# Kernel optimization log

Measured on AMD Instinct MI355X. Metric: run time of the kernel, lower is better.

Reference implementation:

```python
import jax, jax.numpy as jnp
import numpy as np

C = 128; HEADS = 4; DH = C // HEADS; R = 8; EPS = 1e-5; SCALE = DH ** -0.5
B = 1; H = 32; W = 32; D = 32


def _rel_index(r):
    # Faithful replication of RelativePositionBias index (incl. its quirks:
    # depth coord never offset, only coord0 scaled, negative indices wrap).
    coords = np.stack(np.meshgrid(np.arange(r), np.arange(r), np.arange(r), indexing='ij'))
    flat = coords.reshape(3, -1)
    rel = (flat[:, :, None] - flat[:, None, :]).transpose(1, 2, 0).astype(np.int64)
    rel[:, :, 0] += r - 1
    rel[:, :, 1] += r - 1
    rel[:, :, 0] *= 2 * r - 1
    idx = rel.sum(-1)
    tbl = (2 * r - 1) ** 3
    return np.where(idx < 0, idx + tbl, idx)  # torch-style negative index wrap

REL_IDX = jnp.array(_rel_index(R))  # [R^3, R^3]


def _interp_matrix(n_in, n_out):
    # 1-D linear interpolation matrix, align_corners=True (trilinear is separable)
    pos = np.arange(n_out) * (n_in - 1) / (n_out - 1)
    lo = np.clip(np.floor(pos).astype(np.int64), 0, n_in - 2)
    w = (pos - lo).astype(np.float32)
    M = np.zeros((n_out, n_in), np.float32)
    M[np.arange(n_out), lo] = 1.0 - w
    M[np.arange(n_out), lo + 1] += w
    return jnp.array(M)


def _conv3d(x, w, groups=1):
    ks = w.shape[-1]; p = ks // 2
    return jax.lax.conv_general_dilated(
        x, w, (1, 1, 1), ((p, p),) * 3,
        dimension_numbers=('NCDHW', 'OIDHW', 'NCDHW'),
        feature_group_count=groups)


def _bn(x, g, b):
    # training-mode BatchNorm3d: batch stats over (N, spatial), biased var
    mu = x.mean(axis=(0, 2, 3, 4), keepdims=True)
    var = x.var(axis=(0, 2, 3, 4), keepdims=True)
    return (x - mu) * jax.lax.rsqrt(var + EPS) * g.reshape(1, -1, 1, 1, 1) + b.reshape(1, -1, 1, 1, 1)


def _block(x, bn1_g, bn1_b, qkv_dw, qkv_pw, rel_table, out_dw, out_pw, bn2_g, bn2_b, mlp_w):
    Bx, Cx, Hx, Wx, Dx = x.shape
    h = _bn(x, bn1_g, bn1_b)
    qkv = _conv3d(_conv3d(h, qkv_dw, groups=C), qkv_pw)
    q, k, v = jnp.split(qkv, 3, axis=1)
    # trilinear downsample k, v to (R, R, R), align_corners=True
    Mh, Mw, Md = _interp_matrix(Hx, R), _interp_matrix(Wx, R), _interp_matrix(Dx, R)
    k = jnp.einsum('bchwd,ph,qw,rd->bcpqr', k, Mh, Mw, Md)
    v = jnp.einsum('bchwd,ph,qw,rd->bcpqr', v, Mh, Mw, Md)
    # channel layout is (dim_head, heads)
    q = q.reshape(Bx, DH, HEADS, Hx * Wx * Dx).transpose(0, 2, 3, 1)  # b h N d
    k = k.reshape(Bx, DH, HEADS, R ** 3).transpose(0, 2, 3, 1)       # b h M d
    v = v.reshape(Bx, DH, HEADS, R ** 3).transpose(0, 2, 3, 1)
    attn = jnp.einsum('bhid,bhjd->bhij', q, k)
    # relative position bias, expanded by repeat_interleave on each spatial axis
    bias = rel_table[REL_IDX]                          # [R^3, R^3, heads]
    bias = bias.reshape(R, R, R, R ** 3, HEADS)
    ih = jnp.arange(Hx) // (Hx // R)
    iw = jnp.arange(Wx) // (Wx // R)
    idd = jnp.arange(Dx) // (Dx // R)
    bias = bias[ih][:, iw][:, :, idd]                  # [H, W, D, M, heads]
    bias = bias.reshape(Hx * Wx * Dx, R ** 3, HEADS).transpose(2, 0, 1)[None]  # [1, h, N, M]
    attn = (attn + bias) * SCALE                        # scale AFTER bias add, as in source
    attn = jax.nn.softmax(attn, axis=-1)
    out = jnp.einsum('bhij,bhjd->bhid', attn, v)        # b h N d
    out = out.transpose(0, 3, 1, 2).reshape(Bx, C, Hx, Wx, Dx)  # (dim_head heads) channels
    out = _conv3d(_conv3d(out, out_dw, groups=C), out_pw)
    out = out + x
    residue = out
    out = jax.nn.relu(_bn(out, bn2_g, bn2_b))
    out = _conv3d(out, mlp_w)  # 1x1x1, no bias
    return out + residue


def setup_inputs() -> dict:
    key = jax.random.key(0)
    ks = jax.random.split(key, 12)
    s = 0.02
    return {
        'x': jax.random.normal(ks[0], (B, C, H, W, D), jnp.float32),
        'bn1_g': jnp.ones((C,), jnp.float32),
        'bn1_b': jnp.zeros((C,), jnp.float32),
        'qkv_dw': jax.random.normal(ks[1], (C, 1, 3, 3, 3), jnp.float32) * s,
        'qkv_pw': jax.random.normal(ks[2], (3 * C, C, 1, 1, 1), jnp.float32) * s,
        'rel_table': jax.random.normal(ks[3], ((2 * R - 1) ** 3, HEADS), jnp.float32) * s,
        'out_dw': jax.random.normal(ks[4], (C, 1, 3, 3, 3), jnp.float32) * s,
        'out_pw': jax.random.normal(ks[5], (C, C, 1, 1, 1), jnp.float32) * s,
        'bn2_g': jnp.ones((C,), jnp.float32),
        'bn2_b': jnp.zeros((C,), jnp.float32),
        'mlp_w': jax.random.normal(ks[6], (C, C, 1, 1, 1), jnp.float32) * s,
    }


def reference(x, bn1_g, bn1_b, qkv_dw, qkv_pw, rel_table, out_dw, out_pw, bn2_g, bn2_b, mlp_w):
    return _block(x, bn1_g, bn1_b, qkv_dw, qkv_pw, rel_table, out_dw, out_pw, bn2_g, bn2_b, mlp_w)
```

## Files before the change

kernel.cpp:

```cpp
#include <hip/hip_runtime.h>
#include <math.h>


typedef short bf16x8 __attribute__((ext_vector_type(8)));
typedef float f32x4 __attribute__((ext_vector_type(4)));

constexpr int CNUM  = 128;
constexpr int NSP   = 32768;
constexpr int HEADS = 4;
constexpr int M3    = 512;
constexpr float EPSV  = 1e-5f;
constexpr float SCALE = 0.17677669529663688f;
constexpr float SK    = SCALE * 1.44269504088896340736f;

constexpr size_t F_HDW  = 0;
constexpr size_t F_QKV  = 4194304;
constexpr size_t F_Y1   = F_QKV + 4194304;
constexpr size_t F_KD   = 16777216;
constexpr size_t F_VT   = F_KD + 32768;
constexpr size_t F_BIAS = F_VT + 32768;
constexpr size_t F_ST   = F_BIAS + 524288;

__device__ inline ushort f2bf(float f) {
  unsigned u = __float_as_uint(f);
  u += 0x7fff + ((u >> 16) & 1);
  return (ushort)(u >> 16);
}
__device__ inline float bf2f(ushort u) { return __uint_as_float(((unsigned)u) << 16); }

__global__ __launch_bounds__(256) void bn_stats(
    const float* __restrict__ x, const float* __restrict__ g,
    const float* __restrict__ bb, float* __restrict__ scale,
    float* __restrict__ shift) {
  const int c = blockIdx.x;
  const float4* p = (const float4*)(x + (size_t)c * NSP);
  float s = 0.f, s2 = 0.f;
  for (int i = threadIdx.x; i < NSP / 4; i += 256) {
    float4 v = p[i];
    s  += v.x + v.y + v.z + v.w;
    s2 += v.x * v.x + v.y * v.y + v.z * v.z + v.w * v.w;
  }
  __shared__ float rs[4], rs2[4];
  for (int off = 32; off > 0; off >>= 1) {
    s  += __shfl_down(s, off);
    s2 += __shfl_down(s2, off);
  }
  if ((threadIdx.x & 63) == 0) { rs[threadIdx.x >> 6] = s; rs2[threadIdx.x >> 6] = s2; }
  __syncthreads();
  if (threadIdx.x == 0) {
    float S = rs[0] + rs[1] + rs[2] + rs[3];
    float S2 = rs2[0] + rs2[1] + rs2[2] + rs2[3];
    float mu = S / (float)NSP;
    float var = S2 / (float)NSP - mu * mu;
    float sc = g[c] * rsqrtf(var + EPSV);
    scale[c] = sc;
    shift[c] = bb[c] - mu * sc;
  }
}

template <bool AFFINE>
__global__ __launch_bounds__(256) void dwconv3(
    const float* __restrict__ in, const float* __restrict__ w27,
    const float* __restrict__ scale, const float* __restrict__ shift,
    float* __restrict__ out) {
  const int idx = blockIdx.x * 256 + threadIdx.x;
  const int d0 = (idx & 3) << 3;
  const int ww = (idx >> 2) & 31;
  const int hh = (idx >> 7) & 31;
  const int c  = idx >> 12;
  const float sc = AFFINE ? scale[c] : 1.f;
  const float sh = AFFINE ? shift[c] : 0.f;
  const float* pc = in + ((size_t)c << 15);
  const float* wc = w27 + c * 27;
  float wreg[27];
#pragma unroll
  for (int k = 0; k < 27; ++k) wreg[k] = wc[k];

  float acc[8] = {};
#pragma unroll
  for (int a = 0; a < 3; ++a) {
    int h2 = hh + a - 1;
    if ((unsigned)h2 > 31u) continue;
#pragma unroll
    for (int b = 0; b < 3; ++b) {
      int w2 = ww + b - 1;
      if ((unsigned)w2 > 31u) continue;
      const float* row = pc + (h2 << 10) + (w2 << 5) + d0;
      float4 v0 = *(const float4*)(row);
      float4 v1 = *(const float4*)(row + 4);
      float win[10];
      if (AFFINE) {
        win[1] = fmaf(v0.x, sc, sh); win[2] = fmaf(v0.y, sc, sh);
        win[3] = fmaf(v0.z, sc, sh); win[4] = fmaf(v0.w, sc, sh);
        win[5] = fmaf(v1.x, sc, sh); win[6] = fmaf(v1.y, sc, sh);
        win[7] = fmaf(v1.z, sc, sh); win[8] = fmaf(v1.w, sc, sh);
        win[0] = (d0 > 0)  ? fmaf(row[-1], sc, sh) : 0.f;
        win[9] = (d0 < 24) ? fmaf(row[8],  sc, sh) : 0.f;
      } else {
        win[1] = v0.x; win[2] = v0.y; win[3] = v0.z; win[4] = v0.w;
        win[5] = v1.x; win[6] = v1.y; win[7] = v1.z; win[8] = v1.w;
        win[0] = (d0 > 0)  ? row[-1] : 0.f;
        win[9] = (d0 < 24) ? row[8]  : 0.f;
      }
      const float w0 = wreg[(a * 3 + b) * 3 + 0];
      const float w1 = wreg[(a * 3 + b) * 3 + 1];
      const float w2v = wreg[(a * 3 + b) * 3 + 2];
#pragma unroll
      for (int j = 0; j < 8; ++j)
        acc[j] += w0 * win[j] + w1 * win[j + 1] + w2v * win[j + 2];
    }
  }
  float* dst = out + ((size_t)c << 15) + (hh << 10) + (ww << 5) + d0;
  *(float4*)(dst)     = *(float4*)&acc[0];
  *(float4*)(dst + 4) = *(float4*)&acc[4];
}

template <int FUSE>
__global__ __launch_bounds__(256) void gemm128(
    const float* __restrict__ W, const float* __restrict__ Bm,
    const float* __restrict__ res, const float* __restrict__ scale,
    const float* __restrict__ shift, float* __restrict__ out) {
  __shared__ float Wt[64][132];
  __shared__ float Bt[128][68];
  const int tid = threadIdx.x;
  const int bx = blockIdx.x & 511;
  const int by = blockIdx.x >> 9;
  const int n0 = bx << 6, oc0 = by << 6;
  {
    int oc = tid >> 2, f0 = tid & 3;
    const float4* src = (const float4*)(W + (size_t)(oc0 + oc) * 128);
#pragma unroll
    for (int j = 0; j < 8; ++j) {
      float4 v = src[f0 + j * 4];
      *(float4*)&Wt[oc][(f0 + j * 4) * 4] = v;
    }
  }
  {
    int ic = tid >> 1, g0 = tid & 1;
    const float* srcB = Bm + (size_t)ic * NSP + n0;
    float sc = 0.f, sh = 0.f;
    if (FUSE == 2) { sc = scale[ic]; sh = shift[ic]; }
#pragma unroll
    for (int j = 0; j < 8; ++j) {
      float4 v = *(const float4*)(srcB + (g0 + j * 2) * 4);
      if (FUSE == 2) {
        v.x = fmaxf(fmaf(v.x, sc, sh), 0.f);
        v.y = fmaxf(fmaf(v.y, sc, sh), 0.f);
        v.z = fmaxf(fmaf(v.z, sc, sh), 0.f);
        v.w = fmaxf(fmaf(v.w, sc, sh), 0.f);
      }
      *(float4*)&Bt[ic][(g0 + j * 2) * 4] = v;
    }
  }
  __syncthreads();
  const int tx = tid & 15, ty = tid >> 4;
  float acc[4][4] = {};
#pragma unroll 4
  for (int k = 0; k < 128; ++k) {
    float4 bv = *(const float4*)&Bt[k][tx << 2];
    float a[4];
#pragma unroll
    for (int i = 0; i < 4; ++i) a[i] = Wt[(ty << 2) + i][k];
#pragma unroll
    for (int i = 0; i < 4; ++i) {
      acc[i][0] = fmaf(a[i], bv.x, acc[i][0]);
      acc[i][1] = fmaf(a[i], bv.y, acc[i][1]);
      acc[i][2] = fmaf(a[i], bv.z, acc[i][2]);
      acc[i][3] = fmaf(a[i], bv.w, acc[i][3]);
    }
  }
#pragma unroll
  for (int i = 0; i < 4; ++i) {
    int oc = oc0 + (ty << 2) + i;
    float4 o;
    o.x = acc[i][0]; o.y = acc[i][1]; o.z = acc[i][2]; o.w = acc[i][3];
    if (FUSE >= 1) {
      float4 r = *(const float4*)(res + (size_t)oc * NSP + n0 + (tx << 2));
      o.x += r.x; o.y += r.y; o.z += r.z; o.w += r.w;
    }
    *(float4*)(out + (size_t)oc * NSP + n0 + (tx << 2)) = o;
  }
}

__device__ inline void interp8(int p, int& lo, float& w) {
  double pos = (double)p * 31.0 / 7.0;
  int l = (int)pos;
  if (l > 30) l = 30;
  lo = l;
  w = (float)(pos - (double)l);
}

__global__ __launch_bounds__(128) void downsample_kv(
    const float* __restrict__ qkv, ushort* __restrict__ kd,
    ushort* __restrict__ vt) {
  const int m = blockIdx.x, c = threadIdx.x;
  const int p = m >> 6, q = (m >> 3) & 7, r = m & 7;
  int lp, lq, lr; float wp, wq, wr;
  interp8(p, lp, wp); interp8(q, lq, wq); interp8(r, lr, wr);
  const float* kp = qkv + (size_t)(CNUM + c) * NSP;
  const float* vp = qkv + (size_t)(2 * CNUM + c) * NSP;
  float ak = 0.f, av = 0.f;
#pragma unroll
  for (int a = 0; a < 2; ++a)
#pragma unroll
    for (int b = 0; b < 2; ++b)
#pragma unroll
      for (int e = 0; e < 2; ++e) {
        float wgt = (a ? wp : 1.f - wp) * (b ? wq : 1.f - wq) * (e ? wr : 1.f - wr);
        int off = ((lp + a) << 10) + ((lq + b) << 5) + (lr + e);
        ak = fmaf(wgt, kp[off], ak);
        av = fmaf(wgt, vp[off], av);
      }
  const int d = c >> 2, h = c & 3;
  kd[((size_t)(h * M3 + m)) * 32 + d] = f2bf(ak);
  vt[((size_t)(h * 32 + d)) * M3 + m] = f2bf(av);
}

__global__ __launch_bounds__(256) void build_bias(
    const float* __restrict__ rel, ushort* __restrict__ biasmat) {
  const int nr = blockIdx.x;
  const int p0 = nr >> 6, q0 = (nr >> 3) & 7, r0 = nr & 7;
  for (int m = threadIdx.x; m < M3; m += 256) {
    int p1 = m >> 6, q1 = (m >> 3) & 7, r1 = m & 7;
    int idx = (p0 - p1 + 7) * 15 + (q0 - q1 + 7) + (r0 - r1);
    if (idx < 0) idx += 3375;
#pragma unroll
    for (int h = 0; h < 4; ++h)
      biasmat[((size_t)(h * M3 + nr)) * M3 + m] = f2bf(rel[idx * 4 + h]);
  }
}

__global__ __launch_bounds__(256, 2) void attention_mfma(
    const float* __restrict__ q, const ushort* __restrict__ kd,
    const ushort* __restrict__ vt, const ushort* __restrict__ biasg,
    float* __restrict__ attn_out) {
  __shared__ ushort lds[31040];
  ushort* Kl = lds;
  ushort* Vl = lds + 5120;
  ushort* Bl = lds + 9472;
  ushort* Pl = lds + 13632;
  const int tid = threadIdx.x;
  const int lane = tid & 63, w = tid >> 6;
  const int g = lane >> 4, c = lane & 15;
  const int head = blockIdx.x >> 8;
  const int n0 = (blockIdx.x & 255) << 7;

  {
    int nr_base = ((n0 >> 12) << 6) + ((((n0 >> 5) & 31) >> 2) << 3);
    int row = tid >> 5, col = (tid & 31) << 4;
    const float4* src =
        (const float4*)(biasg + ((size_t)(head * M3 + nr_base + row)) * M3 + col);
    *(float4*)&Bl[row * 520 + col] = src[0];
    *(float4*)&Bl[row * 520 + col + 8] = src[1];
  }

  bf16x8 qf[2];
#pragma unroll
  for (int s = 0; s < 2; ++s) {
    int n = n0 + w * 32 + s * 16 + c;
#pragma unroll
    for (int j = 0; j < 8; ++j)
      qf[s][j] = (short)f2bf(q[(size_t)((g * 8 + j) * 4 + head) * NSP + n]);
  }

  f32x4 acc[2][2];
#pragma unroll
  for (int s = 0; s < 2; ++s)
#pragma unroll
    for (int dt = 0; dt < 2; ++dt) acc[s][dt] = {0.f, 0.f, 0.f, 0.f};
  float rmax[2] = {-1e30f, -1e30f};
  float rsum[2] = {0.f, 0.f};
  ushort* Pw = Pl + w * 2 * 2176;
  const f32x4 zero4 = {0.f, 0.f, 0.f, 0.f};

  for (int mt = 0; mt < M3; mt += 128) {
    __syncthreads();
    {
      int r = tid >> 1, hp = (tid & 1) << 4;
      const float4* ksrc =
          (const float4*)(kd + ((size_t)(head * M3 + mt + r)) * 32 + hp);
      *(float4*)&Kl[r * 40 + hp] = ksrc[0];
      *(float4*)&Kl[r * 40 + hp + 8] = ksrc[1];
      int d = tid >> 3, mc = (tid & 7) << 4;
      const float4* vs = (const float4*)(vt + ((size_t)(head * 32 + d)) * M3 + mt + mc);
      *(float4*)&Vl[d * 136 + mc] = vs[0];
      *(float4*)&Vl[d * 136 + mc + 8] = vs[1];
    }
    __syncthreads();
    f32x4 st[2][8];
#pragma unroll
    for (int t = 0; t < 8; ++t) {
      bf16x8 kf = *(const bf16x8*)&Kl[(t * 16 + c) * 40 + g * 8];
      st[0][t] = __builtin_amdgcn_mfma_f32_16x16x32_bf16(kf, qf[0], zero4, 0, 0, 0);
      st[1][t] = __builtin_amdgcn_mfma_f32_16x16x32_bf16(kf, qf[1], zero4, 0, 0, 0);
    }
#pragma unroll
    for (int s = 0; s < 2; ++s) {
      const int brow = s * 4 + (c >> 2);
      float mx = -1e30f;
#pragma unroll
      for (int t = 0; t < 8; ++t) {
        ushort4 bb = *(const ushort4*)&Bl[brow * 520 + mt + t * 16 + g * 4];
        st[s][t][0] = (st[s][t][0] + bf2f(bb.x)) * SK;
        st[s][t][1] = (st[s][t][1] + bf2f(bb.y)) * SK;
        st[s][t][2] = (st[s][t][2] + bf2f(bb.z)) * SK;
        st[s][t][3] = (st[s][t][3] + bf2f(bb.w)) * SK;
        mx = fmaxf(mx, fmaxf(fmaxf(st[s][t][0], st[s][t][1]),
                             fmaxf(st[s][t][2], st[s][t][3])));
      }
      mx = fmaxf(mx, __shfl_xor(mx, 16));
      mx = fmaxf(mx, __shfl_xor(mx, 32));
      float mnew = fmaxf(rmax[s], mx);
      float f = exp2f(rmax[s] - mnew);
      rmax[s] = mnew;
      float psum = 0.f;
      ushort* Ps = Pw + s * 2176;
#pragma unroll
      for (int t = 0; t < 8; ++t) {
        float p0 = exp2f(st[s][t][0] - mnew);
        float p1 = exp2f(st[s][t][1] - mnew);
        float p2 = exp2f(st[s][t][2] - mnew);
        float p3 = exp2f(st[s][t][3] - mnew);
        psum += (p0 + p1) + (p2 + p3);
        ushort4 pw4;
        pw4.x = f2bf(p0); pw4.y = f2bf(p1); pw4.z = f2bf(p2); pw4.w = f2bf(p3);
        *(ushort4*)&Ps[c * 136 + t * 16 + g * 4] = pw4;
      }
      psum += __shfl_xor(psum, 16);
      psum += __shfl_xor(psum, 32);
      rsum[s] = rsum[s] * f + psum;
      float fr0 = __shfl(f, g * 4 + 0), fr1 = __shfl(f, g * 4 + 1);
      float fr2 = __shfl(f, g * 4 + 2), fr3 = __shfl(f, g * 4 + 3);
#pragma unroll
      for (int dt = 0; dt < 2; ++dt) {
        acc[s][dt][0] *= fr0; acc[s][dt][1] *= fr1;
        acc[s][dt][2] *= fr2; acc[s][dt][3] *= fr3;
      }
    }
#pragma unroll
    for (int ks = 0; ks < 4; ++ks) {
      bf16x8 pa0 = *(const bf16x8*)&Pw[c * 136 + ks * 32 + g * 8];
      bf16x8 pa1 = *(const bf16x8*)&Pw[2176 + c * 136 + ks * 32 + g * 8];
#pragma unroll
      for (int dt = 0; dt < 2; ++dt) {
        bf16x8 vb = *(const bf16x8*)&Vl[(dt * 16 + c) * 136 + ks * 32 + g * 8];
        acc[0][dt] = __builtin_amdgcn_mfma_f32_16x16x32_bf16(pa0, vb, acc[0][dt], 0, 0, 0);
        acc[1][dt] = __builtin_amdgcn_mfma_f32_16x16x32_bf16(pa1, vb, acc[1][dt], 0, 0, 0);
      }
    }
  }
  __syncthreads();
  float* Ol = (float*)Pl;
#pragma unroll
  for (int s = 0; s < 2; ++s) {
    float inv = 1.f / rsum[s];
#pragma unroll
    for (int r = 0; r < 4; ++r) {
      float fr = __shfl(inv, g * 4 + r);
      int row = w * 32 + s * 16 + g * 4 + r;
#pragma unroll
      for (int dt = 0; dt < 2; ++dt)
        Ol[row * 33 + dt * 16 + c] = acc[s][dt][r] * fr;
    }
  }
  __syncthreads();
  {
    int d = tid >> 3, seg = tid & 7;
    float vals[16];
#pragma unroll
    for (int i = 0; i < 16; ++i) vals[i] = Ol[(seg * 16 + i) * 33 + d];
    float* dst = attn_out + (size_t)(d * 4 + head) * NSP + n0 + seg * 16;
#pragma unroll
    for (int i = 0; i < 4; ++i) *(float4*)(dst + i * 4) = *(float4*)&vals[i * 4];
  }
}

extern "C" void kernel_launch(void* const* d_in, const int* in_sizes, int n_in,
                              void* d_out, int out_size, void* d_ws, size_t ws_size,
                              hipStream_t stream) {
  (void)in_sizes; (void)n_in; (void)out_size; (void)ws_size;
  const float* x      = (const float*)d_in[0];
  const float* bn1_g  = (const float*)d_in[1];
  const float* bn1_b  = (const float*)d_in[2];
  const float* qkv_dw = (const float*)d_in[3];
  const float* qkv_pw = (const float*)d_in[4];
  const float* rel    = (const float*)d_in[5];
  const float* out_dw = (const float*)d_in[6];
  const float* out_pw = (const float*)d_in[7];
  const float* bn2_g  = (const float*)d_in[8];
  const float* bn2_b  = (const float*)d_in[9];
  const float* mlp_w  = (const float*)d_in[10];
  float* out = (float*)d_out;
  float* ws = (float*)d_ws;

  float* hdw    = ws + F_HDW;
  float* qkv    = ws + F_QKV;
  float* attn_o = ws + F_HDW;
  float* tmp2   = ws + F_QKV;
  float* y1     = ws + F_Y1;
  ushort* kdb   = (ushort*)(ws + F_KD);
  ushort* vtb   = (ushort*)(ws + F_VT);
  ushort* bias  = (ushort*)(ws + F_BIAS);
  float* sc1 = ws + F_ST, *sh1 = sc1 + 128, *sc2 = sh1 + 128, *sh2 = sc2 + 128;

  bn_stats<<<128, 256, 0, stream>>>(x, bn1_g, bn1_b, sc1, sh1);
  dwconv3<true><<<2048, 256, 0, stream>>>(x, qkv_dw, sc1, sh1, hdw);
  gemm128<0><<<512 * 6, 256, 0, stream>>>(qkv_pw, hdw, nullptr, nullptr, nullptr, qkv);
  downsample_kv<<<M3, 128, 0, stream>>>(qkv, kdb, vtb);
  build_bias<<<M3, 256, 0, stream>>>(rel, bias);
  attention_mfma<<<HEADS * 256, 256, 0, stream>>>(qkv, kdb, vtb, bias, attn_o);
  dwconv3<false><<<2048, 256, 0, stream>>>(attn_o, out_dw, nullptr, nullptr, tmp2);
  gemm128<1><<<512 * 2, 256, 0, stream>>>(out_pw, tmp2, x, nullptr, nullptr, y1);
  bn_stats<<<128, 256, 0, stream>>>(y1, bn2_g, bn2_b, sc2, sh2);
  gemm128<2><<<512 * 2, 256, 0, stream>>>(mlp_w, y1, y1, sc2, sh2, out);
}
```

Measured before the change: 297.4 us.

## Replace fp32 pointwise-conv GEMMs with bf16 MFMA GEMMs over transposed activations

The three 1x1x1 convolution GEMMs move from a scalar fp32 FMA kernel to a bf16 MFMA kernel. The depthwise convs now write bf16, and new transpose kernels turn the activations into a spatial-major bf16 layout. The BN2+ReLU affine is folded into the transpose of y1. This cuts ALU-bound GEMM time and halves intermediate traffic, but adds three transpose passes and extra launches and lowers precision to bf16. The GEMM epilogue writes scalars with 16-lane coalescing, which may make those stores less efficient.

```diff
diff --git a/kernel.cpp b/kernel.cpp
--- a/kernel.cpp
+++ b/kernel.cpp
@@ -4,6 +4,7 @@
 
 typedef short bf16x8 __attribute__((ext_vector_type(8)));
 typedef float f32x4 __attribute__((ext_vector_type(4)));
+typedef unsigned short u16x8 __attribute__((ext_vector_type(8)));
 
 constexpr int CNUM  = 128;
 constexpr int NSP   = 32768;
@@ -13,13 +14,18 @@
 constexpr float SCALE = 0.17677669529663688f;
 constexpr float SK    = SCALE * 1.44269504088896340736f;
 
-constexpr size_t F_HDW  = 0;
-constexpr size_t F_QKV  = 4194304;
-constexpr size_t F_Y1   = F_QKV + 4194304;
-constexpr size_t F_KD   = 16777216;
-constexpr size_t F_VT   = F_KD + 32768;
-constexpr size_t F_BIAS = F_VT + 32768;
-constexpr size_t F_ST   = F_BIAS + 524288;
+constexpr size_t F_HDW16 = 0;
+constexpr size_t F_HDWT  = 2097152;
+constexpr size_t F_QKV   = 4194304;
+constexpr size_t F_ATTN  = 0;
+constexpr size_t F_TMP2  = F_QKV;
+constexpr size_t F_TMP2T = F_QKV + 2097152;
+constexpr size_t F_Y1    = F_QKV + 4194304;
+constexpr size_t F_Y1T   = F_QKV + 8388608;
+constexpr size_t F_KD    = 16777216;
+constexpr size_t F_VT    = F_KD + 32768;
+constexpr size_t F_BIAS  = F_VT + 32768;
+constexpr size_t F_ST    = F_BIAS + 524288;
 
 __device__ inline ushort f2bf(float f) {
   unsigned u = __float_as_uint(f);
@@ -62,7 +68,7 @@
 __global__ __launch_bounds__(256) void dwconv3(
     const float* __restrict__ in, const float* __restrict__ w27,
     const float* __restrict__ scale, const float* __restrict__ shift,
-    float* __restrict__ out) {
+    ushort* __restrict__ out) {
   const int idx = blockIdx.x * 256 + threadIdx.x;
   const int d0 = (idx & 3) << 3;
   const int ww = (idx >> 2) & 31;
@@ -110,75 +116,125 @@
         acc[j] += w0 * win[j] + w1 * win[j + 1] + w2v * win[j + 2];
     }
   }
-  float* dst = out + ((size_t)c << 15) + (hh << 10) + (ww << 5) + d0;
-  *(float4*)(dst)     = *(float4*)&acc[0];
-  *(float4*)(dst + 4) = *(float4*)&acc[4];
-}
-
-template <int FUSE>
-__global__ __launch_bounds__(256) void gemm128(
-    const float* __restrict__ W, const float* __restrict__ Bm,
-    const float* __restrict__ res, const float* __restrict__ scale,
-    const float* __restrict__ shift, float* __restrict__ out) {
-  __shared__ float Wt[64][132];
-  __shared__ float Bt[128][68];
+  u16x8 o;
+#pragma unroll
+  for (int j = 0; j < 8; ++j) o[j] = f2bf(acc[j]);
+  *(u16x8*)(out + ((size_t)c << 15) + (hh << 10) + (ww << 5) + d0) = o;
+}
+
+template <int MODE>
+__global__ __launch_bounds__(256) void transpose_cn(
+    const void* __restrict__ inp, const float* __restrict__ sc_,
+    const float* __restrict__ sh_, ushort* __restrict__ outp) {
+  __shared__ ushort T[64][72];
   const int tid = threadIdx.x;
-  const int bx = blockIdx.x & 511;
-  const int by = blockIdx.x >> 9;
-  const int n0 = bx << 6, oc0 = by << 6;
-  {
-    int oc = tid >> 2, f0 = tid & 3;
-    const float4* src = (const float4*)(W + (size_t)(oc0 + oc) * 128);
-#pragma unroll
-    for (int j = 0; j < 8; ++j) {
-      float4 v = src[f0 + j * 4];
-      *(float4*)&Wt[oc][(f0 + j * 4) * 4] = v;
-    }
-  }
-  {
-    int ic = tid >> 1, g0 = tid & 1;
-    const float* srcB = Bm + (size_t)ic * NSP + n0;
-    float sc = 0.f, sh = 0.f;
-    if (FUSE == 2) { sc = scale[ic]; sh = shift[ic]; }
-#pragma unroll
-    for (int j = 0; j < 8; ++j) {
-      float4 v = *(const float4*)(srcB + (g0 + j * 2) * 4);
-      if (FUSE == 2) {
-        v.x = fmaxf(fmaf(v.x, sc, sh), 0.f);
-        v.y = fmaxf(fmaf(v.y, sc, sh), 0.f);
-        v.z = fmaxf(fmaf(v.z, sc, sh), 0.f);
-        v.w = fmaxf(fmaf(v.w, sc, sh), 0.f);
-      }
-      *(float4*)&Bt[ic][(g0 + j * 2) * 4] = v;
-    }
+  const int c0 = (blockIdx.x & 1) << 6;
+  const int n0 = (blockIdx.x >> 1) << 6;
+  const int r = tid >> 2, q = (tid & 3) << 4;
+  if (MODE == 0) {
+    const ushort* src = (const ushort*)inp + (size_t)(c0 + r) * NSP + n0 + q;
+    *(u16x8*)&T[r][q]     = *(const u16x8*)src;
+    *(u16x8*)&T[r][q + 8] = *(const u16x8*)(src + 8);
+  } else {
+    const float* src = (const float*)inp + (size_t)(c0 + r) * NSP + n0 + q;
+    const float s = sc_[c0 + r], h = sh_[c0 + r];
+    float4 v0 = ((const float4*)src)[0], v1 = ((const float4*)src)[1];
+    float4 v2 = ((const float4*)src)[2], v3 = ((const float4*)src)[3];
+    u16x8 a, b;
+    a[0] = f2bf(fmaxf(fmaf(v0.x, s, h), 0.f));
+    a[1] = f2bf(fmaxf(fmaf(v0.y, s, h), 0.f));
+    a[2] = f2bf(fmaxf(fmaf(v0.z, s, h), 0.f));
+    a[3] = f2bf(fmaxf(fmaf(v0.w, s, h), 0.f));
+    a[4] = f2bf(fmaxf(fmaf(v1.x, s, h), 0.f));
+    a[5] = f2bf(fmaxf(fmaf(v1.y, s, h), 0.f));
+    a[6] = f2bf(fmaxf(fmaf(v1.z, s, h), 0.f));
+    a[7] = f2bf(fmaxf(fmaf(v1.w, s, h), 0.f));
+    b[0] = f2bf(fmaxf(fmaf(v2.x, s, h), 0.f));
+    b[1] = f2bf(fmaxf(fmaf(v2.y, s, h), 0.f));
+    b[2] = f2bf(fmaxf(fmaf(v2.z, s, h), 0.f));
+    b[3] = f2bf(fmaxf(fmaf(v2.w, s, h), 0.f));
+    b[4] = f2bf(fmaxf(fmaf(v3.x, s, h), 0.f));
+    b[5] = f2bf(fmaxf(fmaf(v3.y, s, h), 0.f));
+    b[6] = f2bf(fmaxf(fmaf(v3.z, s, h), 0.f));
+    b[7] = f2bf(fmaxf(fmaf(v3.w, s, h), 0.f));
+    *(u16x8*)&T[r][q]     = a;
+    *(u16x8*)&T[r][q + 8] = b;
   }
   __syncthreads();
-  const int tx = tid & 15, ty = tid >> 4;
-  float acc[4][4] = {};
-#pragma unroll 4
-  for (int k = 0; k < 128; ++k) {
-    float4 bv = *(const float4*)&Bt[k][tx << 2];
-    float a[4];
-#pragma unroll
-    for (int i = 0; i < 4; ++i) a[i] = Wt[(ty << 2) + i][k];
-#pragma unroll
-    for (int i = 0; i < 4; ++i) {
-      acc[i][0] = fmaf(a[i], bv.x, acc[i][0]);
-      acc[i][1] = fmaf(a[i], bv.y, acc[i][1]);
-      acc[i][2] = fmaf(a[i], bv.z, acc[i][2]);
-      acc[i][3] = fmaf(a[i], bv.w, acc[i][3]);
-    }
-  }
-#pragma unroll
-  for (int i = 0; i < 4; ++i) {
-    int oc = oc0 + (ty << 2) + i;
-    float4 o;
-    o.x = acc[i][0]; o.y = acc[i][1]; o.z = acc[i][2]; o.w = acc[i][3];
-    if (FUSE >= 1) {
-      float4 r = *(const float4*)(res + (size_t)oc * NSP + n0 + (tx << 2));
-      o.x += r.x; o.y += r.y; o.z += r.z; o.w += r.w;
-    }
-    *(float4*)(out + (size_t)oc * NSP + n0 + (tx << 2)) = o;
+  const int rn = tid >> 2, cq = (tid & 3) << 4;
+  u16x8 o0, o1;
+#pragma unroll
+  for (int j = 0; j < 8; ++j) { o0[j] = T[cq + j][rn]; o1[j] = T[cq + 8 + j][rn]; }
+  ushort* dst = outp + (size_t)(n0 + rn) * 128 + c0 + cq;
+  *(u16x8*)dst       = o0;
+  *(u16x8*)(dst + 8) = o1;
+}
+
+template <bool RES>
+__global__ __launch_bounds__(256) void gemm_mfma(
+    const float* __restrict__ W, const ushort* __restrict__ Bt,
+    const float* __restrict__ res, float* __restrict__ out) {
+  __shared__ ushort Wl[128][40];
+  __shared__ ushort Bl[128][40];
+  const int tid = threadIdx.x;
+  const int lane = tid & 63, w = tid >> 6;
+  const int g = lane >> 4, c = lane & 15;
+  const int n0 = blockIdx.x << 7, oc0 = blockIdx.y << 7;
+  const int wr = (w >> 1) << 6, wc = (w & 1) << 6;
+  f32x4 acc[4][4];
+#pragma unroll
+  for (int mt = 0; mt < 4; ++mt)
+#pragma unroll
+    for (int nt = 0; nt < 4; ++nt) acc[mt][nt] = {0.f, 0.f, 0.f, 0.f};
+  const int sr = tid >> 1, sh2 = (tid & 1) << 4;
+  for (int k0 = 0; k0 < 128; k0 += 32) {
+    __syncthreads();
+    {
+      const float* wsrc = W + (size_t)(oc0 + sr) * 128 + k0 + sh2;
+      float4 a = ((const float4*)wsrc)[0];
+      float4 b = ((const float4*)wsrc)[1];
+      float4 cc = ((const float4*)wsrc)[2];
+      float4 dd = ((const float4*)wsrc)[3];
+      u16x8 p0, p1;
+      p0[0] = f2bf(a.x);  p0[1] = f2bf(a.y);  p0[2] = f2bf(a.z);  p0[3] = f2bf(a.w);
+      p0[4] = f2bf(b.x);  p0[5] = f2bf(b.y);  p0[6] = f2bf(b.z);  p0[7] = f2bf(b.w);
+      p1[0] = f2bf(cc.x); p1[1] = f2bf(cc.y); p1[2] = f2bf(cc.z); p1[3] = f2bf(cc.w);
+      p1[4] = f2bf(dd.x); p1[5] = f2bf(dd.y); p1[6] = f2bf(dd.z); p1[7] = f2bf(dd.w);
+      *(u16x8*)&Wl[sr][sh2]     = p0;
+      *(u16x8*)&Wl[sr][sh2 + 8] = p1;
+      const ushort* bsrc = Bt + (size_t)(n0 + sr) * 128 + k0 + sh2;
+      *(u16x8*)&Bl[sr][sh2]     = *(const u16x8*)bsrc;
+      *(u16x8*)&Bl[sr][sh2 + 8] = *(const u16x8*)(bsrc + 8);
+    }
+    __syncthreads();
+    bf16x8 af[4], bfr[4];
+#pragma unroll
+    for (int mt = 0; mt < 4; ++mt)
+      af[mt] = *(const bf16x8*)&Wl[wr + mt * 16 + c][g * 8];
+#pragma unroll
+    for (int nt = 0; nt < 4; ++nt)
+      bfr[nt] = *(const bf16x8*)&Bl[wc + nt * 16 + c][g * 8];
+#pragma unroll
+    for (int mt = 0; mt < 4; ++mt)
+#pragma unroll
+      for (int nt = 0; nt < 4; ++nt)
+        acc[mt][nt] = __builtin_amdgcn_mfma_f32_16x16x32_bf16(
+            af[mt], bfr[nt], acc[mt][nt], 0, 0, 0);
+  }
+#pragma unroll
+  for (int mt = 0; mt < 4; ++mt) {
+#pragma unroll
+    for (int nt = 0; nt < 4; ++nt) {
+      const int n = n0 + wc + nt * 16 + c;
+#pragma unroll
+      for (int r = 0; r < 4; ++r) {
+        const int oc = oc0 + wr + mt * 16 + g * 4 + r;
+        size_t off = (size_t)oc * NSP + n;
+        float o = acc[mt][nt][r];
+        if (RES) o += res[off];
+        out[off] = o;
+      }
+    }
   }
 }
 
@@ -393,24 +449,30 @@
   float* out = (float*)d_out;
   float* ws = (float*)d_ws;
 
-  float* hdw    = ws + F_HDW;
-  float* qkv    = ws + F_QKV;
-  float* attn_o = ws + F_HDW;
-  float* tmp2   = ws + F_QKV;
-  float* y1     = ws + F_Y1;
+  ushort* hdw16 = (ushort*)(ws + F_HDW16);
+  ushort* hdwt  = (ushort*)(ws + F_HDWT);
+  float*  qkv   = ws + F_QKV;
+  float*  attn_o = ws + F_ATTN;
+  ushort* tmp2  = (ushort*)(ws + F_TMP2);
+  ushort* tmp2t = (ushort*)(ws + F_TMP2T);
+  float*  y1    = ws + F_Y1;
+  ushort* y1t   = (ushort*)(ws + F_Y1T);
   ushort* kdb   = (ushort*)(ws + F_KD);
   ushort* vtb   = (ushort*)(ws + F_VT);
   ushort* bias  = (ushort*)(ws + F_BIAS);
   float* sc1 = ws + F_ST, *sh1 = sc1 + 128, *sc2 = sh1 + 128, *sh2 = sc2 + 128;
 
   bn_stats<<<128, 256, 0, stream>>>(x, bn1_g, bn1_b, sc1, sh1);
-  dwconv3<true><<<2048, 256, 0, stream>>>(x, qkv_dw, sc1, sh1, hdw);
-  gemm128<0><<<512 * 6, 256, 0, stream>>>(qkv_pw, hdw, nullptr, nullptr, nullptr, qkv);
+  dwconv3<true><<<2048, 256, 0, stream>>>(x, qkv_dw, sc1, sh1, hdw16);
+  transpose_cn<0><<<1024, 256, 0, stream>>>(hdw16, nullptr, nullptr, hdwt);
+  gemm_mfma<false><<<dim3(256, 3), 256, 0, stream>>>(qkv_pw, hdwt, nullptr, qkv);
   downsample_kv<<<M3, 128, 0, stream>>>(qkv, kdb, vtb);
   build_bias<<<M3, 256, 0, stream>>>(rel, bias);
   attention_mfma<<<HEADS * 256, 256, 0, stream>>>(qkv, kdb, vtb, bias, attn_o);
   dwconv3<false><<<2048, 256, 0, stream>>>(attn_o, out_dw, nullptr, nullptr, tmp2);
-  gemm128<1><<<512 * 2, 256, 0, stream>>>(out_pw, tmp2, x, nullptr, nullptr, y1);
+  transpose_cn<0><<<1024, 256, 0, stream>>>(tmp2, nullptr, nullptr, tmp2t);
+  gemm_mfma<true><<<dim3(256, 1), 256, 0, stream>>>(out_pw, tmp2t, x, y1);
   bn_stats<<<128, 256, 0, stream>>>(y1, bn2_g, bn2_b, sc2, sh2);
-  gemm128<2><<<512 * 2, 256, 0, stream>>>(mlp_w, y1, y1, sc2, sh2, out);
-}
+  transpose_cn<1><<<1024, 256, 0, stream>>>(y1, sc2, sh2, y1t);
+  gemm_mfma<true><<<dim3(256, 1), 256, 0, stream>>>(mlp_w, y1t, y1, out);
+}
```

Result: faster. 262.5 us (-11.8%).
